# Kernel optimization log

Hardware: AMD Instinct MI355X
Metric: run time of the kernel (lower is better)

Reference implementation:

```python
import jax, jax.numpy as jnp
import numpy as np

B, PLEN, D = 32, 1024, 256


def setup_inputs() -> dict:
    key = jax.random.key(0)
    ks = jax.random.split(key, 8)
    u = lambda k, shape: jax.random.uniform(k, shape, jnp.float32, -0.05, 0.05)
    return {
        "P": jax.random.normal(ks[0], (B, PLEN, D), jnp.float32),
        "w_itr_att": u(ks[1], (3 * D,)),
        "w1": u(ks[2], (2 * D, D)),
        "w2": u(ks[3], (2 * D, D)),
        "w3": u(ks[4], (2 * D, D)),
        "b1": u(ks[5], (D,)),
        "b2": u(ks[6], (D,)),
        "b3": u(ks[7], (D,)),
    }


def reference(P, w_itr_att, w1, w2, w3, b1, b2, b3):
    d = P.shape[-1]
    # alpha(a,b) = w_itr_att . [a ; b ; a*b]; split w into the three d-chunks
    wa, wb, wc = w_itr_att[:d], w_itr_att[d:2 * d], w_itr_att[2 * d:]
    # pairwise score A[b,i,j] = wa.P_i + wb.P_j + wc.(P_i * P_j)
    sa = P @ wa                                   # (b, p)
    sb = P @ wb                                   # (b, p)
    A = sa[:, :, None] + sb[:, None, :] + jnp.einsum('bid,bjd->bij', P * wc, P)
    itr_attn = jnp.einsum('bij,bjd->bid', jax.nn.softmax(A, axis=2), P)
    cat = jnp.concatenate([P, itr_attn], axis=-1)  # (b, p, 2d)
    z = jnp.tanh(cat @ w1 + b1)
    r = jax.nn.sigmoid(cat @ w2 + b2)
    f = jax.nn.sigmoid(cat @ w3 + b3)
    return r * P + f * z
```

## Files before the change

kernel.cpp:

```cpp
#include <hip/hip_runtime.h>
#include <hip/hip_bf16.h>

typedef unsigned short u16;
typedef unsigned int   u32;

using bf16x8 = __attribute__((ext_vector_type(8))) short;
using f32x4  = __attribute__((ext_vector_type(4))) float;

#define NB 32
#define NP 1024
#define ND 256

__device__ __forceinline__ u16 f2bf(float x){
  u32 u = __float_as_uint(x);
  u += 0x7FFFu + ((u >> 16) & 1u);
  return (u16)(u >> 16);
}

__device__ __forceinline__ float bf2f(u16 x){
  return __uint_as_float((u32)x << 16);
}

__device__ __forceinline__ void glds16(const void* g, void* l){
  __builtin_amdgcn_global_load_lds((const __attribute__((address_space(1))) void*)g,
                                   (__attribute__((address_space(3))) void*)l, 16, 0, 0);
}

__global__ void prep_rows(const float* __restrict__ P, const float* __restrict__ wi,
                          u16* __restrict__ Pbf, float* __restrict__ sbv){
  const int row  = blockIdx.x * 4 + (threadIdx.x >> 6);
  const int lane = threadIdx.x & 63;
  const float4 p  = *(const float4*)(P  + (size_t)row * ND + lane * 4);
  const float4 wb = *(const float4*)(wi + ND + lane * 4);
  ushort4 pb;
  pb.x = f2bf(p.x); pb.y = f2bf(p.y); pb.z = f2bf(p.z); pb.w = f2bf(p.w);
  *(ushort4*)(Pbf + (size_t)row * ND + lane * 4) = pb;
  float s = p.x*wb.x + p.y*wb.y + p.z*wb.z + p.w*wb.w;
  #pragma unroll
  for (int m = 1; m < 64; m <<= 1) s += __shfl_xor(s, m, 64);
  if (lane == 0) sbv[row] = s;
}

__global__ void prep_w(const float* __restrict__ w1, const float* __restrict__ w2,
                       const float* __restrict__ w3, u16* __restrict__ Wp){
  const int t = blockIdx.x;
  const float* w = (t < 16) ? w1 : ((t < 32) ? w2 : w3);
  const int tid = threadIdx.x;
  #pragma unroll
  for (int j = 0; j < 4; ++j){
    int item = tid + 256 * j;
    int c = item >> 6, lane = item & 63;
    int ncol = ((t & 15) << 4) + (lane & 15);
    int k0 = 32 * c + 8 * (lane >> 4);
    u16 tmp[8];
    #pragma unroll
    for (int e = 0; e < 8; ++e) tmp[e] = f2bf(w[(size_t)(k0 + e) * 256 + ncol]);
    *(uint4*)(Wp + ((size_t)(t * 16 + c) * 64 + lane) * 8) = *(uint4*)tmp;
  }
}

__global__ void transpose_p(const u16* __restrict__ Pbf, u16* __restrict__ PbfT){
  const int b = blockIdx.z, jt = blockIdx.x, dt = blockIdx.y;
  __shared__ u16 T[64][72];
  const int tid = threadIdx.x;
  #pragma unroll
  for (int it = 0; it < 2; ++it){
    int cc = tid + 256 * it;
    int j = cc >> 3, c8 = cc & 7;
    uint4 v = *(const uint4*)(Pbf + ((size_t)b * NP + jt * 64 + j) * ND + dt * 64 + c8 * 8);
    *(uint4*)&T[j][c8 * 8] = v;
  }
  __syncthreads();
  #pragma unroll
  for (int it = 0; it < 2; ++it){
    int cc = tid + 256 * it;
    int d = cc >> 3, c8 = cc & 7;
    u16 tmp[8];
    #pragma unroll
    for (int k = 0; k < 8; ++k) tmp[k] = T[c8 * 8 + k][d];
    *(uint4*)(PbfT + ((size_t)b * ND + dt * 64 + d) * NP + jt * 64 + c8 * 8) = *(uint4*)tmp;
  }
}

__launch_bounds__(256, 3)
__global__ void attn_kernel(const float* __restrict__ P, const float* __restrict__ wi,
                            const u16* __restrict__ Pbf, const u16* __restrict__ PbfT,
                            const float* __restrict__ sbv, u16* __restrict__ attnb){
  const int p    = blockIdx.x;
  const int bid  = ((p & 7) << 6) | (p >> 3);
  const int b    = bid >> 4;
  const int q0   = (bid & 15) << 6;
  const int tid  = threadIdx.x;
  const int wave = tid >> 6, lane = tid & 63, lo = lane & 15, hi = lane >> 4;

  __shared__ __align__(16) u16 KtA[32 * 256];
  __shared__ __align__(16) u16 VtA[256 * 32];
  __shared__ __align__(16) u16 Sp[4][16][40];
  char* KtB = (char*)KtA;
  char* VtB = (char*)VtA;

  bf16x8 qf[8];
  {
    const int qrow = q0 + wave * 16 + lo;
    const float* prow = P  + ((size_t)b * NP + qrow) * ND;
    const float* wcp  = wi + 512;
    #pragma unroll
    for (int c = 0; c < 8; ++c){
      const int d0 = 32 * c + 8 * hi;
      float4 a  = *(const float4*)(prow + d0);
      float4 a2 = *(const float4*)(prow + d0 + 4);
      float4 wa  = *(const float4*)(wcp + d0);
      float4 wa2 = *(const float4*)(wcp + d0 + 4);
      bf16x8 q;
      q[0]=(short)f2bf(a.x*wa.x);  q[1]=(short)f2bf(a.y*wa.y);
      q[2]=(short)f2bf(a.z*wa.z);  q[3]=(short)f2bf(a.w*wa.w);
      q[4]=(short)f2bf(a2.x*wa2.x); q[5]=(short)f2bf(a2.y*wa2.y);
      q[6]=(short)f2bf(a2.z*wa2.z); q[7]=(short)f2bf(a2.w*wa2.w);
      qf[c] = q;
    }
  }

  f32x4 of[16];
  #pragma unroll
  for (int t = 0; t < 16; ++t) of[t] = (f32x4){0.f,0.f,0.f,0.f};
  float mx[4] = {-1e30f,-1e30f,-1e30f,-1e30f};
  float ls[4] = {0.f,0.f,0.f,0.f};

  const u16* kslab = Pbf  + (size_t)b * NP * ND;
  const u16* vslab = PbfT + (size_t)b * ND * NP;

  auto stageK = [&](int kt){
    const int kbase = kt * 32;
    #pragma unroll
    for (int it = 0; it < 4; ++it){
      int off = it * 4096 + tid * 16;
      int j   = off >> 9;
      int ck  = ((off >> 4) & 31) ^ (j & 7);
      glds16((const char*)(kslab + (size_t)(kbase + j) * ND + ck * 8), KtB + off);
    }
  };
  auto stageV = [&](int kt){
    const int kbase = kt * 32;
    #pragma unroll
    for (int it = 0; it < 4; ++it){
      int off = it * 4096 + tid * 16;
      int pidx = off >> 4;
      int d   = pidx >> 2;
      int u   = pidx & 3;
      int kc  = u ^ ((d >> 1) & 3);
      glds16((const char*)(vslab + (size_t)d * NP + kbase + kc * 8), VtB + off);
    }
  };

  float sbc[2], sbn[2];
  stageK(0);
  stageV(0);
  #pragma unroll
  for (int nt = 0; nt < 2; ++nt) sbc[nt] = sbv[(size_t)b * NP + nt * 16 + lo];
  __syncthreads();

  for (int kt = 0; kt < 32; ++kt){
    f32x4 s[2];
    #pragma unroll
    for (int nt = 0; nt < 2; ++nt){
      f32x4 acc = (f32x4){0.f,0.f,0.f,0.f};
      #pragma unroll
      for (int c = 0; c < 8; ++c){
        int j  = nt * 16 + lo;
        int ad = j * 512 + (((4 * c + hi) ^ (j & 7)) << 4);
        bf16x8 kf = *(const bf16x8*)(KtB + ad);
        acc = __builtin_amdgcn_mfma_f32_16x16x32_bf16(qf[c], kf, acc, 0, 0, 0);
      }
      s[nt] = acc;
      float sv = sbc[nt];
      #pragma unroll
      for (int r = 0; r < 4; ++r) s[nt][r] += sv;
    }

    __syncthreads();
    if (kt < 31) stageK(kt + 1);

    float md = -1e30f;
    #pragma unroll
    for (int nt = 0; nt < 2; ++nt)
      #pragma unroll
      for (int r = 0; r < 4; ++r) md = fmaxf(md, s[nt][r] - mx[r]);
    if (!__all(md <= 8.f)){
      float scale[4];
      #pragma unroll
      for (int r = 0; r < 4; ++r){
        float v = fmaxf(s[0][r], s[1][r]);
        v = fmaxf(v, __shfl_xor(v, 1, 64));
        v = fmaxf(v, __shfl_xor(v, 2, 64));
        v = fmaxf(v, __shfl_xor(v, 4, 64));
        v = fmaxf(v, __shfl_xor(v, 8, 64));
        float mnew = fmaxf(mx[r], v);
        scale[r] = __expf(mx[r] - mnew);
        mx[r] = mnew;
        ls[r] *= scale[r];
      }
      #pragma unroll
      for (int t = 0; t < 16; ++t)
        #pragma unroll
        for (int r = 0; r < 4; ++r) of[t][r] *= scale[r];
    }
    #pragma unroll
    for (int nt = 0; nt < 2; ++nt)
      #pragma unroll
      for (int r = 0; r < 4; ++r){
        float pv = __expf(s[nt][r] - mx[r]);
        ls[r] += pv;
        Sp[wave][4 * hi + r][16 * nt + lo] = f2bf(pv);
      }

    {
      bf16x8 pa = *(const bf16x8*)&Sp[wave][lo][8 * hi];
      #pragma unroll
      for (int t = 0; t < 16; ++t){
        int d  = 16 * t + lo;
        int ad = d * 64 + ((hi ^ ((d >> 1) & 3)) << 4);
        bf16x8 vb = *(const bf16x8*)(VtB + ad);
        of[t] = __builtin_amdgcn_mfma_f32_16x16x32_bf16(pa, vb, of[t], 0, 0, 0);
      }
    }

    __syncthreads();
    if (kt < 31){
      stageV(kt + 1);
      #pragma unroll
      for (int nt = 0; nt < 2; ++nt)
        sbn[nt] = sbv[(size_t)b * NP + (kt + 1) * 32 + nt * 16 + lo];
      sbc[0] = sbn[0]; sbc[1] = sbn[1];
    }
  }

  #pragma unroll
  for (int r = 0; r < 4; ++r){
    ls[r] += __shfl_xor(ls[r], 1, 64);
    ls[r] += __shfl_xor(ls[r], 2, 64);
    ls[r] += __shfl_xor(ls[r], 4, 64);
    ls[r] += __shfl_xor(ls[r], 8, 64);
  }
  const int qrow = q0 + wave * 16;
  #pragma unroll
  for (int t = 0; t < 16; ++t){
    #pragma unroll
    for (int r = 0; r < 4; ++r){
      float o = of[t][r] / ls[r];
      attnb[((size_t)b * NP + qrow + 4 * hi + r) * ND + 16 * t + lo] = f2bf(o);
    }
  }
}

__launch_bounds__(256, 2)
__global__ void mlp_kernel(const u16* __restrict__ Pbf, const u16* __restrict__ attnb,
                           const u16* __restrict__ Wp,
                           const float* __restrict__ b1, const float* __restrict__ b2,
                           const float* __restrict__ b3, float* __restrict__ out){
  const int p    = blockIdx.x;
  const int swz  = ((p & 7) << 7) | (p >> 3);
  const int mt   = swz >> 2, cg = swz & 3;
  const int tid  = threadIdx.x;
  const int wave = tid >> 6, lane = tid & 63, lo = lane & 15, hi = lane >> 4;
  const int tq   = 4 * cg + wave;
  const int m0   = mt * 128;

  __shared__ __align__(16) u16 Ab[2][128 * 64];

  f32x4 acc[3][8];
  #pragma unroll
  for (int e = 0; e < 3; ++e)
    #pragma unroll
    for (int m = 0; m < 8; ++m) acc[e][m] = (f32x4){0.f,0.f,0.f,0.f};

  auto stage = [&](int s, int buf){
    const u16* xs = (s < 4) ? (Pbf   + (size_t)m0 * ND + s * 64)
                            : (attnb + (size_t)m0 * ND + (s - 4) * 64);
    char* dst = (char*)Ab[buf];
    #pragma unroll
    for (int it = 0; it < 4; ++it){
      int off = it * 4096 + wave * 1024 + lane * 16;
      int row = off >> 7;
      int cl  = (off & 127) ^ ((row & 7) << 4);
      glds16((const char*)(xs + (size_t)row * ND) + cl, dst + it * 4096 + wave * 1024);
    }
  };

  stage(0, 0);
  __syncthreads();

  for (int s = 0; s < 8; ++s){
    if (s < 7) stage(s + 1, (s + 1) & 1);
    const char* ab = (const char*)Ab[s & 1];
    #pragma unroll
    for (int cc = 0; cc < 2; ++cc){
      const int c = 2 * s + cc;
      bf16x8 wf[3];
      #pragma unroll
      for (int e = 0; e < 3; ++e)
        wf[e] = *(const bf16x8*)(Wp + ((size_t)((tq + 16 * e) * 16 + c) * 64 + lane) * 8);
      #pragma unroll
      for (int m = 0; m < 8; ++m){
        int row = 16 * m + lo;
        bf16x8 af = *(const bf16x8*)(ab + row * 128 + ((64 * cc + 16 * hi) ^ ((row & 7) << 4)));
        #pragma unroll
        for (int e = 0; e < 3; ++e)
          acc[e][m] = __builtin_amdgcn_mfma_f32_16x16x32_bf16(af, wf[e], acc[e][m], 0, 0, 0);
      }
    }
    __syncthreads();
  }

  const int d = 16 * tq + lo;
  const float bb1 = b1[d], bb2 = b2[d], bb3 = b3[d];
  #pragma unroll
  for (int m = 0; m < 8; ++m){
    #pragma unroll
    for (int r = 0; r < 4; ++r){
      const int row = m0 + 16 * m + 4 * hi + r;
      float y1 = acc[0][m][r] + bb1;
      float y2 = acc[1][m][r] + bb2;
      float y3 = acc[2][m][r] + bb3;
      float pv = bf2f(Pbf[(size_t)row * ND + d]);
      float e2 = __expf(2.f * y1);
      float z  = (e2 - 1.f) / (e2 + 1.f);
      float rr = 1.f / (1.f + __expf(-y2));
      float ff = 1.f / (1.f + __expf(-y3));
      out[(size_t)row * ND + d] = rr * pv + ff * z;
    }
  }
}

extern "C" void kernel_launch(void* const* d_in, const int* in_sizes, int n_in,
                              void* d_out, int out_size, void* d_ws, size_t ws_size,
                              hipStream_t stream){
  const float* P  = (const float*)d_in[0];
  const float* wi = (const float*)d_in[1];
  const float* w1 = (const float*)d_in[2];
  const float* w2 = (const float*)d_in[3];
  const float* w3 = (const float*)d_in[4];
  const float* b1 = (const float*)d_in[5];
  const float* b2 = (const float*)d_in[6];
  const float* b3 = (const float*)d_in[7];
  float* out = (float*)d_out;

  char* ws = (char*)d_ws;
  u16*   Pbf   = (u16*)  (ws);
  u16*   PbfT  = (u16*)  (ws + (16u << 20));
  u16*   attnb = (u16*)  (ws + (32u << 20));
  u16*   Wp    = (u16*)  (ws + (48u << 20));
  float* sbv   = (float*)(ws + (49u << 20));

  prep_rows<<<8192, 256, 0, stream>>>(P, wi, Pbf, sbv);
  prep_w<<<48, 256, 0, stream>>>(w1, w2, w3, Wp);
  transpose_p<<<dim3(16, 4, 32), 256, 0, stream>>>(Pbf, PbfT);
  attn_kernel<<<512, 256, 0, stream>>>(P, wi, Pbf, PbfT, sbv, attnb);
  mlp_kernel<<<1024, 256, 0, stream>>>(Pbf, attnb, Wp, b1, b2, b3, out);
}
```

Measured before the change: 124.3 us.

## Split attention key range across two blocks and merge with combine kernel

Each query tile's key loop is split into two halves handled by separate blocks, doubling the grid from 512 to 1024 blocks. Each half writes a bf16 partial output plus its per-row max and sum, and a new combine kernel rescales and merges the two halves. The goal is better CU occupancy on a grid that was too small to fill the device. The cost is an extra kernel launch, extra global traffic for the partial buffers, and a second bf16 rounding of the output. The path is only taken when the workspace is large enough.

```diff
diff --git a/kernel.cpp b/kernel.cpp
--- a/kernel.cpp
+++ b/kernel.cpp
@@ -85,9 +85,23 @@
 __launch_bounds__(256, 3)
 __global__ void attn_kernel(const float* __restrict__ P, const float* __restrict__ wi,
                             const u16* __restrict__ Pbf, const u16* __restrict__ PbfT,
-                            const float* __restrict__ sbv, u16* __restrict__ attnb){
-  const int p    = blockIdx.x;
-  const int bid  = ((p & 7) << 6) | (p >> 3);
+                            const float* __restrict__ sbv,
+                            u16* __restrict__ ob0, u16* __restrict__ ob1,
+                            float* __restrict__ mlb, int splitk){
+  int p2, kt0, nkt;
+  u16* obuf;
+  float* mlo;
+  if (splitk){
+    const int half = blockIdx.x >> 9;
+    p2  = blockIdx.x & 511;
+    kt0 = half * 16; nkt = 16;
+    obuf = half ? ob1 : ob0;
+    mlo  = mlb + (size_t)half * 2 * (NB * NP);
+  } else {
+    p2 = blockIdx.x; kt0 = 0; nkt = 32;
+    obuf = ob0; mlo = nullptr;
+  }
+  const int bid  = ((p2 & 7) << 6) | (p2 >> 3);
   const int b    = bid >> 4;
   const int q0   = (bid & 15) << 6;
   const int tid  = threadIdx.x;
@@ -153,13 +167,14 @@
   };
 
   float sbc[2], sbn[2];
-  stageK(0);
-  stageV(0);
-  #pragma unroll
-  for (int nt = 0; nt < 2; ++nt) sbc[nt] = sbv[(size_t)b * NP + nt * 16 + lo];
+  stageK(kt0);
+  stageV(kt0);
+  #pragma unroll
+  for (int nt = 0; nt < 2; ++nt) sbc[nt] = sbv[(size_t)b * NP + kt0 * 32 + nt * 16 + lo];
   __syncthreads();
 
-  for (int kt = 0; kt < 32; ++kt){
+  for (int kk = 0; kk < nkt; ++kk){
+    const int kt = kt0 + kk;
     f32x4 s[2];
     #pragma unroll
     for (int nt = 0; nt < 2; ++nt){
@@ -178,7 +193,7 @@
     }
 
     __syncthreads();
-    if (kt < 31) stageK(kt + 1);
+    if (kk < nkt - 1) stageK(kt + 1);
 
     float md = -1e30f;
     #pragma unroll
@@ -225,7 +240,7 @@
     }
 
     __syncthreads();
-    if (kt < 31){
+    if (kk < nkt - 1){
       stageV(kt + 1);
       #pragma unroll
       for (int nt = 0; nt < 2; ++nt)
@@ -247,9 +262,41 @@
     #pragma unroll
     for (int r = 0; r < 4; ++r){
       float o = of[t][r] / ls[r];
-      attnb[((size_t)b * NP + qrow + 4 * hi + r) * ND + 16 * t + lo] = f2bf(o);
-    }
-  }
+      obuf[((size_t)b * NP + qrow + 4 * hi + r) * ND + 16 * t + lo] = f2bf(o);
+    }
+  }
+  if (mlo && lo == 0){
+    #pragma unroll
+    for (int r = 0; r < 4; ++r){
+      size_t rowi = (size_t)b * NP + qrow + 4 * hi + r;
+      mlo[2 * rowi]     = mx[r];
+      mlo[2 * rowi + 1] = ls[r];
+    }
+  }
+}
+
+__global__ void combine_kernel(const u16* __restrict__ o2buf,
+                               const float* __restrict__ mlb,
+                               u16* __restrict__ attnb){
+  const int tid = threadIdx.x;
+  const size_t row = (size_t)blockIdx.x * 8 + (tid >> 5);
+  const int d0 = (tid & 31) * 8;
+  const float m1 = mlb[2 * row],                l1 = mlb[2 * row + 1];
+  const float m2 = mlb[2 * (NB * NP) + 2 * row], l2 = mlb[2 * (NB * NP) + 2 * row + 1];
+  const float m  = fmaxf(m1, m2);
+  const float w1 = __expf(m1 - m) * l1;
+  const float w2 = __expf(m2 - m) * l2;
+  const float inv = 1.f / (w1 + w2);
+  const float a1 = w1 * inv, a2 = w2 * inv;
+  uint4 v1 = *(const uint4*)(attnb + row * ND + d0);
+  uint4 v2 = *(const uint4*)(o2buf + row * ND + d0);
+  const u16* p1 = (const u16*)&v1;
+  const u16* p2 = (const u16*)&v2;
+  u16 outv[8];
+  #pragma unroll
+  for (int e = 0; e < 8; ++e)
+    outv[e] = f2bf(a1 * bf2f(p1[e]) + a2 * bf2f(p2[e]));
+  *(uint4*)(attnb + row * ND + d0) = *(uint4*)outv;
 }
 
 __launch_bounds__(256, 2)
@@ -350,10 +397,16 @@
   u16*   attnb = (u16*)  (ws + (32u << 20));
   u16*   Wp    = (u16*)  (ws + (48u << 20));
   float* sbv   = (float*)(ws + (49u << 20));
+  u16*   part1 = (u16*)  (ws + (50u << 20));
+  float* mlb   = (float*)(ws + (66u << 20));
+
+  const int splitk = (ws_size >= (67ull << 20)) ? 1 : 0;
 
   prep_rows<<<8192, 256, 0, stream>>>(P, wi, Pbf, sbv);
   prep_w<<<48, 256, 0, stream>>>(w1, w2, w3, Wp);
   transpose_p<<<dim3(16, 4, 32), 256, 0, stream>>>(Pbf, PbfT);
-  attn_kernel<<<512, 256, 0, stream>>>(P, wi, Pbf, PbfT, sbv, attnb);
+  attn_kernel<<<splitk ? 1024 : 512, 256, 0, stream>>>(P, wi, Pbf, PbfT, sbv,
+                                                       attnb, part1, mlb, splitk);
+  if (splitk) combine_kernel<<<4096, 256, 0, stream>>>(part1, mlb, attnb);
   mlp_kernel<<<1024, 256, 0, stream>>>(Pbf, attnb, Wp, b1, b2, b3, out);
 }
```

Measured after the change: 141.4 us. 1.14x slower.
